# Kernel tuning notes

Measured on AMD Instinct MI355X. Metric: run time of the kernel, lower is better.

Reference implementation:

```python
import jax, jax.numpy as jnp
import numpy as np

INPUT_SIZE = 128
HIDDEN_SIZE = 128
BATCH = 65536


def _xavier(key, shape):
    fan_out, fan_in = shape
    limit = np.sqrt(6.0 / (fan_in + fan_out)).astype(np.float32)
    return jax.random.uniform(key, shape, jnp.float32, -limit, limit)


def setup_inputs() -> dict:
    key = jax.random.key(0)
    ks = jax.random.split(key, 12)
    inp = {
        "x": jax.random.normal(ks[0], (BATCH, INPUT_SIZE), jnp.float32),
        "h_t": jax.random.normal(ks[1], (BATCH, HIDDEN_SIZE), jnp.float32),
        "c_t": jax.random.normal(ks[2], (BATCH, HIDDEN_SIZE), jnp.float32),
        "W_ii": _xavier(ks[3], (HIDDEN_SIZE, INPUT_SIZE)),
        "W_hi": _xavier(ks[4], (HIDDEN_SIZE, HIDDEN_SIZE)),
        "b_i": jnp.zeros((HIDDEN_SIZE,), jnp.float32),
        "W_if": _xavier(ks[5], (HIDDEN_SIZE, INPUT_SIZE)),
        "W_hf": _xavier(ks[6], (HIDDEN_SIZE, HIDDEN_SIZE)),
        "b_f": jnp.zeros((HIDDEN_SIZE,), jnp.float32),
        "W_ig": _xavier(ks[7], (HIDDEN_SIZE, INPUT_SIZE)),
        "W_hg": _xavier(ks[8], (HIDDEN_SIZE, HIDDEN_SIZE)),
        "b_g": jnp.zeros((HIDDEN_SIZE,), jnp.float32),
        "W_io": _xavier(ks[9], (HIDDEN_SIZE, INPUT_SIZE)),
        "W_ho": _xavier(ks[10], (HIDDEN_SIZE, HIDDEN_SIZE)),
        "b_o": jnp.zeros((HIDDEN_SIZE,), jnp.float32),
    }
    return inp


def reference(x, h_t, c_t, W_ii, W_hi, b_i, W_if, W_hf, b_f, W_ig, W_hg, b_g, W_io, W_ho, b_o):
    # Fuse the 8 small GEMMs into 2 concatenated GEMMs, identical math to
    # per-gate F.linear calls (same weights, just stacked along output dim).
    W_x = jnp.concatenate([W_ii, W_if, W_ig, W_io], axis=0)   # [4H, I]
    W_h = jnp.concatenate([W_hi, W_hf, W_hg, W_ho], axis=0)   # [4H, H]
    b = jnp.concatenate([b_i, b_f, b_g, b_o], axis=0)         # [4H]
    gates = x @ W_x.T + h_t @ W_h.T + b                       # [B, 4H]
    i_a, f_a, g_a, o_a = jnp.split(gates, 4, axis=1)
    i_t = jax.nn.sigmoid(i_a)
    f_t = jax.nn.sigmoid(f_a)
    g_t = jnp.tanh(g_a)
    o_t = jax.nn.sigmoid(o_a)
    c_new = f_t * c_t + i_t * g_t
    h_new = o_t * jnp.tanh(c_new)
    return (h_new, c_new)
```

## Files before the change

kernel.cpp:

```cpp
#include <hip/hip_runtime.h>
#include <hip/hip_bf16.h>


typedef short s16x8 __attribute__((ext_vector_type(8)));
typedef float f32x4 __attribute__((ext_vector_type(4)));

__device__ __forceinline__ short f2bf(float f) {
    __hip_bfloat16 h = __float2bfloat16(f);
    return __builtin_bit_cast(short, h);
}
__device__ __forceinline__ float sigm(float x) { return 1.0f / (1.0f + __expf(-x)); }
__device__ __forceinline__ float tanh_f(float x) { return 1.0f - 2.0f / (1.0f + __expf(2.0f * x)); }

__global__ __launch_bounds__(256)
void repack_weights(const float* __restrict__ Wii, const float* __restrict__ Whi,
                    const float* __restrict__ Wif, const float* __restrict__ Whf,
                    const float* __restrict__ Wig, const float* __restrict__ Whg,
                    const float* __restrict__ Wio, const float* __restrict__ Who,
                    short* __restrict__ ws)
{
    const int t     = blockIdx.x * 256 + threadIdx.x;
    const int chunk = t >> 6;
    const int l     = t & 63;
    const int ks    = chunk & 3;
    const int half  = (chunk >> 2) & 1;
    const int g     = (chunk >> 3) & 3;
    const int wn    = (chunk >> 5) & 1;
    const int jt    = chunk >> 6;
    const int j     = jt * 32 + wn * 16 + (l & 15);
    const int k0    = (ks * 4 + (l >> 4)) * 8;

    const float* wp;
    if (half == 0) wp = (g == 0) ? Wii : (g == 1) ? Wif : (g == 2) ? Wig : Wio;
    else           wp = (g == 0) ? Whi : (g == 1) ? Whf : (g == 2) ? Whg : Who;

    const float* src = wp + (size_t)j * 128 + k0;
    f32x4 a = *(const f32x4*)src;
    f32x4 b = *(const f32x4*)(src + 4);
    s16x8 v;
#pragma unroll
    for (int k = 0; k < 4; ++k) { v[k] = f2bf(a[k]); v[4 + k] = f2bf(b[k]); }
    *(s16x8*)(ws + (size_t)t * 8) = v;
}

__global__ __launch_bounds__(256, 3)
void lstm_cell_kernel(const float* __restrict__ X,
                      const float* __restrict__ H,
                      const float* __restrict__ C,
                      const float* __restrict__ Bi, const float* __restrict__ Bf,
                      const float* __restrict__ Bg, const float* __restrict__ Bo,
                      const short* __restrict__ WS,
                      float* __restrict__ OutH,
                      float* __restrict__ OutC)
{
    __shared__ short sA[128 * 128];

    const int tid = threadIdx.x;
    const int l  = tid & 63;
    const int w  = tid >> 6;
    const int wm = w & 1;
    const int wn = w >> 1;
    const int lj = l & 15;
    const int lq = l >> 4;

    const int jt = blockIdx.x & 3;
    const int bb = blockIdx.x >> 2;
    const int B0 = bb * 128;
    const int J0 = jt * 32;

    f32x4 acc[4][4];
#pragma unroll
    for (int mt = 0; mt < 4; ++mt)
#pragma unroll
        for (int g = 0; g < 4; ++g)
            acc[mt][g] = (f32x4){0.f, 0.f, 0.f, 0.f};

    const short* wsbase = WS + ((size_t)(jt * 2 + wn) * 32) * 512 + l * 8;

#pragma unroll
    for (int half = 0; half < 2; ++half) {
        const float* Asrc = half ? H : X;

        s16x8 bfh[4][4];
#pragma unroll
        for (int g = 0; g < 4; ++g)
#pragma unroll
            for (int ks = 0; ks < 4; ++ks)
                bfh[g][ks] = *(const s16x8*)(wsbase + (size_t)((g * 2 + half) * 4 + ks) * 512);

#pragma unroll
        for (int tt = 0; tt < 2; ++tt) {
            f32x4 f[4][2];
#pragma unroll
            for (int t = 0; t < 4; ++t) {
                const int cc   = (tt * 4 + t) * 256 + tid;
                const int m    = cc >> 4;
                const int oct  = cc & 15;
                const int soct = oct ^ (m & 15);
                const float* src = Asrc + (size_t)(B0 + m) * 128 + soct * 8;
                f[t][0] = *(const f32x4*)src;
                f[t][1] = *(const f32x4*)(src + 4);
            }
#pragma unroll
            for (int t = 0; t < 4; ++t) {
                const int cc = (tt * 4 + t) * 256 + tid;
                s16x8 v;
#pragma unroll
                for (int k = 0; k < 4; ++k) {
                    v[k]     = f2bf(f[t][0][k]);
                    v[4 + k] = f2bf(f[t][1][k]);
                }
                *(s16x8*)(sA + cc * 8) = v;
            }
        }
        __syncthreads();

#pragma unroll
        for (int ks = 0; ks < 4; ++ks) {
            const int oct = (ks * 4 + lq) ^ lj;
            s16x8 af[4];
#pragma unroll
            for (int mt = 0; mt < 4; ++mt) {
                const int m = wm * 64 + mt * 16 + lj;
                af[mt] = *(const s16x8*)(sA + m * 128 + oct * 8);
            }
#pragma unroll
            for (int mt = 0; mt < 4; ++mt)
#pragma unroll
                for (int g = 0; g < 4; ++g)
                    acc[mt][g] = __builtin_amdgcn_mfma_f32_16x16x32_bf16(
                        af[mt], bfh[g][ks], acc[mt][g], 0, 0, 0);
        }
        __syncthreads();
    }

    const int j = J0 + wn * 16 + lj;
    const float bi  = Bi[j];
    const float bfv = Bf[j];
    const float bg  = Bg[j];
    const float bo  = Bo[j];

#pragma unroll
    for (int mt = 0; mt < 4; ++mt) {
#pragma unroll
        for (int r = 0; r < 4; ++r) {
            const int b   = B0 + wm * 64 + mt * 16 + lq * 4 + r;
            const size_t idx = (size_t)b * 128 + j;
            const float ia = acc[mt][0][r] + bi;
            const float fa = acc[mt][1][r] + bfv;
            const float ga = acc[mt][2][r] + bg;
            const float oa = acc[mt][3][r] + bo;
            const float it = sigm(ia);
            const float ft = sigm(fa);
            const float gt = tanh_f(ga);
            const float ot = sigm(oa);
            const float co = C[idx];
            const float cn = ft * co + it * gt;
            const float hn = ot * tanh_f(cn);
            OutH[idx] = hn;
            OutC[idx] = cn;
        }
    }
}

extern "C" void kernel_launch(void* const* d_in, const int* in_sizes, int n_in,
                              void* d_out, int out_size, void* d_ws, size_t ws_size,
                              hipStream_t stream) {
    const float* X   = (const float*)d_in[0];
    const float* H   = (const float*)d_in[1];
    const float* C   = (const float*)d_in[2];
    const float* Wii = (const float*)d_in[3];
    const float* Whi = (const float*)d_in[4];
    const float* Bi  = (const float*)d_in[5];
    const float* Wif = (const float*)d_in[6];
    const float* Whf = (const float*)d_in[7];
    const float* Bf  = (const float*)d_in[8];
    const float* Wig = (const float*)d_in[9];
    const float* Whg = (const float*)d_in[10];
    const float* Bg  = (const float*)d_in[11];
    const float* Wio = (const float*)d_in[12];
    const float* Who = (const float*)d_in[13];
    const float* Bo  = (const float*)d_in[14];

    short* ws = (short*)d_ws;

    hipLaunchKernelGGL(repack_weights, dim3(64), dim3(256), 0, stream,
                       Wii, Whi, Wif, Whf, Wig, Whg, Wio, Who, ws);

    float* OutH = (float*)d_out;
    float* OutC = OutH + (size_t)65536 * 128;

    hipLaunchKernelGGL(lstm_cell_kernel, dim3(2048), dim3(256), 0, stream,
                       X, H, C, Bi, Bf, Bg, Bo, ws, OutH, OutC);
}
```

Measured before the change: 197.7 us.

## Drop LDS staging; load A fragments directly from global per wave

Removes the shared-memory tile and both barriers. Each wave now owns 32 rows and all 32 output columns (8 N-tiles covering 4 gates × 2 halves), loading the X/H fragments straight from global memory into MFMA registers and streaming the weight fragments per k-step. Block indices are remapped so that the 4 column tiles of a row block sit 8 blocks apart, to improve L2 reuse of the activations. The trade is uncoalesced 32-byte row segments in the global loads and a weight reload every k-step, in exchange for no LDS traffic and no synchronisation.

```diff
diff --git a/kernel.cpp b/kernel.cpp
--- a/kernel.cpp
+++ b/kernel.cpp
@@ -25,9 +25,9 @@
     const int ks    = chunk & 3;
     const int half  = (chunk >> 2) & 1;
     const int g     = (chunk >> 3) & 3;
-    const int wn    = (chunk >> 5) & 1;
+    const int jh    = (chunk >> 5) & 1;
     const int jt    = chunk >> 6;
-    const int j     = jt * 32 + wn * 16 + (l & 15);
+    const int j     = jt * 32 + jh * 16 + (l & 15);
     const int k0    = (ks * 4 + (l >> 4)) * 8;
 
     const float* wp;
@@ -53,112 +53,88 @@
                       float* __restrict__ OutH,
                       float* __restrict__ OutC)
 {
-    __shared__ short sA[128 * 128];
-
     const int tid = threadIdx.x;
     const int l  = tid & 63;
-    const int w  = tid >> 6;
-    const int wm = w & 1;
-    const int wn = w >> 1;
+    const int wv = tid >> 6;
     const int lj = l & 15;
     const int lq = l >> 4;
 
-    const int jt = blockIdx.x & 3;
-    const int bb = blockIdx.x >> 2;
+    const unsigned u  = blockIdx.x;
+    const int jt = (u >> 3) & 3;
+    const int bb = (int)(((u >> 5) << 3) | (u & 7));
     const int B0 = bb * 128;
     const int J0 = jt * 32;
+    const int R0 = B0 + wv * 32;
 
-    f32x4 acc[4][4];
+    f32x4 acc[2][8];
 #pragma unroll
-    for (int mt = 0; mt < 4; ++mt)
+    for (int mt = 0; mt < 2; ++mt)
 #pragma unroll
-        for (int g = 0; g < 4; ++g)
-            acc[mt][g] = (f32x4){0.f, 0.f, 0.f, 0.f};
+        for (int nt = 0; nt < 8; ++nt)
+            acc[mt][nt] = (f32x4){0.f, 0.f, 0.f, 0.f};
 
-    const short* wsbase = WS + ((size_t)(jt * 2 + wn) * 32) * 512 + l * 8;
+    const short* wq = WS + (size_t)jt * 32768 + l * 8;
 
 #pragma unroll
     for (int half = 0; half < 2; ++half) {
         const float* Asrc = half ? H : X;
-
-        s16x8 bfh[4][4];
 #pragma unroll
-        for (int g = 0; g < 4; ++g)
+        for (int ks = 0; ks < 4; ++ks) {
+            s16x8 af[2];
 #pragma unroll
-            for (int ks = 0; ks < 4; ++ks)
-                bfh[g][ks] = *(const s16x8*)(wsbase + (size_t)((g * 2 + half) * 4 + ks) * 512);
+            for (int mt = 0; mt < 2; ++mt) {
+                const int row = R0 + mt * 16 + lj;
+                const float* src = Asrc + (size_t)row * 128 + ks * 32 + lq * 8;
+                f32x4 a = *(const f32x4*)src;
+                f32x4 b = *(const f32x4*)(src + 4);
+#pragma unroll
+                for (int k = 0; k < 4; ++k) {
+                    af[mt][k]     = f2bf(a[k]);
+                    af[mt][4 + k] = f2bf(b[k]);
+                }
+            }
+            s16x8 bf[8];
+#pragma unroll
+            for (int nt = 0; nt < 8; ++nt) {
+                const int jh = nt & 1, g = nt >> 1;
+                bf[nt] = *(const s16x8*)(wq + (size_t)(jh * 32 + g * 8 + half * 4 + ks) * 512);
+            }
+#pragma unroll
+            for (int mt = 0; mt < 2; ++mt)
+#pragma unroll
+                for (int nt = 0; nt < 8; ++nt)
+                    acc[mt][nt] = __builtin_amdgcn_mfma_f32_16x16x32_bf16(
+                        af[mt], bf[nt], acc[mt][nt], 0, 0, 0);
+        }
+    }
 
 #pragma unroll
-        for (int tt = 0; tt < 2; ++tt) {
-            f32x4 f[4][2];
+    for (int jh = 0; jh < 2; ++jh) {
+        const int j = J0 + jh * 16 + lj;
+        const float bi  = Bi[j];
+        const float bfv = Bf[j];
+        const float bg  = Bg[j];
+        const float bo  = Bo[j];
 #pragma unroll
-            for (int t = 0; t < 4; ++t) {
-                const int cc   = (tt * 4 + t) * 256 + tid;
-                const int m    = cc >> 4;
-                const int oct  = cc & 15;
-                const int soct = oct ^ (m & 15);
-                const float* src = Asrc + (size_t)(B0 + m) * 128 + soct * 8;
-                f[t][0] = *(const f32x4*)src;
-                f[t][1] = *(const f32x4*)(src + 4);
+        for (int mt = 0; mt < 2; ++mt) {
+#pragma unroll
+            for (int r = 0; r < 4; ++r) {
+                const int b = R0 + mt * 16 + lq * 4 + r;
+                const size_t idx = (size_t)b * 128 + j;
+                const float ia = acc[mt][0 * 2 + jh][r] + bi;
+                const float fa = acc[mt][1 * 2 + jh][r] + bfv;
+                const float ga = acc[mt][2 * 2 + jh][r] + bg;
+                const float oa = acc[mt][3 * 2 + jh][r] + bo;
+                const float it = sigm(ia);
+                const float ft = sigm(fa);
+                const float gt = tanh_f(ga);
+                const float ot = sigm(oa);
+                const float co = C[idx];
+                const float cn = ft * co + it * gt;
+                const float hn = ot * tanh_f(cn);
+                OutH[idx] = hn;
+                OutC[idx] = cn;
             }
-#pragma unroll
-            for (int t = 0; t < 4; ++t) {
-                const int cc = (tt * 4 + t) * 256 + tid;
-                s16x8 v;
-#pragma unroll
-                for (int k = 0; k < 4; ++k) {
-                    v[k]     = f2bf(f[t][0][k]);
-                    v[4 + k] = f2bf(f[t][1][k]);
-                }
-                *(s16x8*)(sA + cc * 8) = v;
-            }
-        }
-        __syncthreads();
-
-#pragma unroll
-        for (int ks = 0; ks < 4; ++ks) {
-            const int oct = (ks * 4 + lq) ^ lj;
-            s16x8 af[4];
-#pragma unroll
-            for (int mt = 0; mt < 4; ++mt) {
-                const int m = wm * 64 + mt * 16 + lj;
-                af[mt] = *(const s16x8*)(sA + m * 128 + oct * 8);
-            }
-#pragma unroll
-            for (int mt = 0; mt < 4; ++mt)
-#pragma unroll
-                for (int g = 0; g < 4; ++g)
-                    acc[mt][g] = __builtin_amdgcn_mfma_f32_16x16x32_bf16(
-                        af[mt], bfh[g][ks], acc[mt][g], 0, 0, 0);
-        }
-        __syncthreads();
-    }
-
-    const int j = J0 + wn * 16 + lj;
-    const float bi  = Bi[j];
-    const float bfv = Bf[j];
-    const float bg  = Bg[j];
-    const float bo  = Bo[j];
-
-#pragma unroll
-    for (int mt = 0; mt < 4; ++mt) {
-#pragma unroll
-        for (int r = 0; r < 4; ++r) {
-            const int b   = B0 + wm * 64 + mt * 16 + lq * 4 + r;
-            const size_t idx = (size_t)b * 128 + j;
-            const float ia = acc[mt][0][r] + bi;
-            const float fa = acc[mt][1][r] + bfv;
-            const float ga = acc[mt][2][r] + bg;
-            const float oa = acc[mt][3][r] + bo;
-            const float it = sigm(ia);
-            const float ft = sigm(fa);
-            const float gt = tanh_f(ga);
-            const float ot = sigm(oa);
-            const float co = C[idx];
-            const float cn = ft * co + it * gt;
-            const float hn = ot * tanh_f(cn);
-            OutH[idx] = hn;
-            OutC[idx] = cn;
         }
     }
 }
```

After: 232.5 us. 17.6% more time.
